# Kernel tuning notes

Hardware: AMD Instinct MI355X
Metric: run time of the kernel (lower is better)

Reference implementation:

```python
import jax, jax.numpy as jnp
import numpy as np

B, S, H = 2, 2048, 2048
NH, NKV, HD = 16, 4, 128          # query heads, kv heads, head_dim
THETA = 10000.0


def setup_inputs() -> dict:
    key = jax.random.key(0)
    ks = jax.random.split(key, 9)
    s = 0.02
    return {
        "hidden_states": jax.random.normal(ks[0], (B, S, H), jnp.float32),
        "q_w": jax.random.normal(ks[1], (NH * HD, H), jnp.float32) * s,
        "q_b": jax.random.normal(ks[2], (NH * HD,), jnp.float32) * s,
        "k_w": jax.random.normal(ks[3], (NKV * HD, H), jnp.float32) * s,
        "k_b": jax.random.normal(ks[4], (NKV * HD,), jnp.float32) * s,
        "v_w": jax.random.normal(ks[5], (NKV * HD, H), jnp.float32) * s,
        "v_b": jax.random.normal(ks[6], (NKV * HD,), jnp.float32) * s,
        "o_w": jax.random.normal(ks[7], (H, NH * HD), jnp.float32) * s,
        "o_b": jax.random.normal(ks[8], (H,), jnp.float32) * s,
    }


def _rotate_half(x):
    x1, x2 = jnp.split(x, 2, axis=-1)
    return jnp.concatenate([-x2, x1], axis=-1)


def reference(hidden_states, q_w, q_b, k_w, k_b, v_w, v_b, o_w, o_b):
    b, s, h = hidden_states.shape
    # QKV projections -> (b, heads, s, hd)
    q = (hidden_states @ q_w.T + q_b).reshape(b, s, NH, HD).transpose(0, 2, 1, 3)
    k = (hidden_states @ k_w.T + k_b).reshape(b, s, NKV, HD).transpose(0, 2, 1, 3)
    v = (hidden_states @ v_w.T + v_b).reshape(b, s, NKV, HD).transpose(0, 2, 1, 3)
    # rotary embedding (default position_ids = arange(s))
    pos = jnp.arange(s, dtype=jnp.float32)
    inv_freq = 1.0 / (THETA ** (jnp.arange(0, HD, 2, dtype=jnp.float32) / HD))
    freqs = pos[:, None] * inv_freq[None, :]          # (s, hd/2)
    emb = jnp.concatenate([freqs, freqs], axis=-1)    # (s, hd)
    cos = jnp.cos(emb)[None, None]                    # (1,1,s,hd)
    sin = jnp.sin(emb)[None, None]
    q = q * cos + _rotate_half(q) * sin
    k = k * cos + _rotate_half(k) * sin
    # GQA: repeat kv heads (repeat_interleave along head dim)
    n_rep = NH // NKV
    k = jnp.repeat(k, n_rep, axis=1)
    v = jnp.repeat(v, n_rep, axis=1)
    # attention (mathematically what the chunked online-softmax intends)
    scores = jnp.einsum('bhqd,bhkd->bhqk', q, k) / np.sqrt(HD).astype(np.float32)
    m = jnp.max(scores, axis=-1, keepdims=True)
    e = jnp.exp(scores - m)
    attn = jnp.einsum('bhqk,bhkd->bhqd', e, v) / (jnp.sum(e, axis=-1, keepdims=True) + 1e-10)
    attn = attn.transpose(0, 2, 1, 3).reshape(b, s, NH * HD)
    return attn @ o_w.T + o_b
```

## Files before the change

kernel.cpp:

```cpp
#include <hip/hip_runtime.h>
#include <hip/hip_bf16.h>
#include <math.h>

typedef __attribute__((ext_vector_type(8))) short bf16x8;
typedef __attribute__((ext_vector_type(4))) float f32x4;
typedef __attribute__((ext_vector_type(16))) float f32x16;
typedef __attribute__((ext_vector_type(4))) unsigned int u32x4;

#if __has_builtin(__builtin_amdgcn_exp2f)
#define EXP2(x) __builtin_amdgcn_exp2f(x)
#else
#define EXP2(x) __expf((x) * 0.6931471805599453f)
#endif

__device__ __forceinline__ ushort f2bf(float f) {
  unsigned u = __float_as_uint(f);
  u = u + 0x7FFFu + ((u >> 16) & 1u);
  return (ushort)(u >> 16);
}
__device__ __forceinline__ float bf2f(ushort h) {
  return __uint_as_float(((unsigned)h) << 16);
}
__device__ __forceinline__ unsigned cvtpk(float a, float b) {
  unsigned r;
  asm("v_cvt_pk_bf16_f32 %0, %1, %2" : "=v"(r) : "v"(a), "v"(b));
  return r;
}
__device__ __forceinline__ void gload_lds16(const ushort* g, ushort* l) {
  __builtin_amdgcn_global_load_lds((const __attribute__((address_space(1))) void*)g,
                                   (__attribute__((address_space(3))) void*)l, 16, 0, 0);
}

__global__ __launch_bounds__(256) void prep_kernel(
    const float* __restrict__ hs, const float* __restrict__ qw,
    const float* __restrict__ kw, const float* __restrict__ vw,
    const float* __restrict__ ow, const float* __restrict__ qb,
    const float* __restrict__ kb, const float* __restrict__ vb,
    ushort* __restrict__ hs_b, ushort* __restrict__ qkvw_b,
    ushort* __restrict__ ow_b, float* __restrict__ qkvb)
{
  const int idx = blockIdx.x * 256 + threadIdx.x;
  const int stride = gridDim.x * 256;
  const float4* hs4 = (const float4*)hs;
  const float4* qw4 = (const float4*)qw;
  const float4* kw4 = (const float4*)kw;
  const float4* vw4 = (const float4*)vw;
  const float4* ow4 = (const float4*)ow;
  ushort4* hsb4 = (ushort4*)hs_b;
  ushort4* qkvwb4 = (ushort4*)qkvw_b;
  ushort4* owb4 = (ushort4*)ow_b;

  for (int i = idx; i < 2097152; i += stride) {
    float4 v = hs4[i];
    ushort4 o; o.x=f2bf(v.x); o.y=f2bf(v.y); o.z=f2bf(v.z); o.w=f2bf(v.w);
    hsb4[i] = o;
  }
  for (int i = idx; i < 1048576; i += stride) {
    float4 v = qw4[i];
    ushort4 o; o.x=f2bf(v.x); o.y=f2bf(v.y); o.z=f2bf(v.z); o.w=f2bf(v.w);
    qkvwb4[i] = o;
  }
  for (int i = idx; i < 262144; i += stride) {
    float4 v = kw4[i];
    ushort4 o; o.x=f2bf(v.x); o.y=f2bf(v.y); o.z=f2bf(v.z); o.w=f2bf(v.w);
    qkvwb4[1048576 + i] = o;
  }
  for (int i = idx; i < 262144; i += stride) {
    float4 v = vw4[i];
    ushort4 o; o.x=f2bf(v.x); o.y=f2bf(v.y); o.z=f2bf(v.z); o.w=f2bf(v.w);
    qkvwb4[1310720 + i] = o;
  }
  for (int i = idx; i < 1048576; i += stride) {
    float4 v = ow4[i];
    ushort4 o; o.x=f2bf(v.x); o.y=f2bf(v.y); o.z=f2bf(v.z); o.w=f2bf(v.w);
    owb4[i] = o;
  }
  for (int i = idx; i < 3072; i += stride)
    qkvb[i] = (i < 2048) ? qb[i] : (i < 2560 ? kb[i - 2048] : vb[i - 2560]);
}

template<int BF16OUT>
__global__ __launch_bounds__(256) void gemm_bt(
    const ushort* __restrict__ A, const ushort* __restrict__ Bw,
    const float* __restrict__ bias, void* __restrict__ Cout,
    ushort* __restrict__ vt,
    int M, int N, int K, int ldc, int vsplit)
{
  __shared__ ushort As[128 * 32];
  __shared__ ushort Bs[128 * 32];
  const int t = threadIdx.x;
  const int wv = t >> 6;
  const int lane = t & 63;
  const int qd = lane >> 4, ln = lane & 15;
  const long row0 = (long)blockIdx.x * 128, col0 = (long)blockIdx.y * 128;
  const int wm = (wv >> 1) * 64, wn = (wv & 1) * 64;

  f32x4 acc[4][4];
#pragma unroll
  for (int i = 0; i < 4; i++)
#pragma unroll
    for (int j = 0; j < 4; j++) acc[i][j] = (f32x4){0.f, 0.f, 0.f, 0.f};

  const ushort* gA = A + (row0 + (t >> 2)) * (long)K + (t & 3) * 8;
  const ushort* gB = Bw + (col0 + (t >> 2)) * (long)K + (t & 3) * 8;
  ushort* lA = &As[wv * 512];
  ushort* lB = &Bs[wv * 512];
  const long K64 = 64l * K;

  for (int kt = 0; kt < K; kt += 32) {
    __syncthreads();
    gload_lds16(gA + kt,        lA);
    gload_lds16(gA + kt + K64,  lA + 2048);
    gload_lds16(gB + kt,        lB);
    gload_lds16(gB + kt + K64,  lB + 2048);
    __syncthreads();
    bf16x8 af[4], bf[4];
#pragma unroll
    for (int mi = 0; mi < 4; mi++)
      af[mi] = *(const bf16x8*)&As[(wm + mi * 16 + ln) * 32 + qd * 8];
#pragma unroll
    for (int ni = 0; ni < 4; ni++)
      bf[ni] = *(const bf16x8*)&Bs[(wn + ni * 16 + ln) * 32 + qd * 8];
#pragma unroll
    for (int mi = 0; mi < 4; mi++)
#pragma unroll
      for (int ni = 0; ni < 4; ni++)
        acc[mi][ni] = __builtin_amdgcn_mfma_f32_16x16x32_bf16(af[mi], bf[ni], acc[mi][ni], 0, 0, 0);
  }

  float bv[4];
#pragma unroll
  for (int ni = 0; ni < 4; ni++) bv[ni] = bias[col0 + wn + ni * 16 + ln];

  if (col0 >= vsplit) {
#pragma unroll
    for (int mi = 0; mi < 4; mi++)
#pragma unroll
      for (int ni = 0; ni < 4; ni++)
#pragma unroll
        for (int r = 0; r < 4; r++) {
          long row = row0 + wm + mi * 16 + qd * 4 + r;
          long col = col0 + wn + ni * 16 + ln - vsplit;
          vt[col * 4096 + row] = f2bf(acc[mi][ni][r] + bv[ni]);
        }
  } else {
#pragma unroll
    for (int mi = 0; mi < 4; mi++)
#pragma unroll
      for (int ni = 0; ni < 4; ni++)
#pragma unroll
        for (int r = 0; r < 4; r++) {
          long row = row0 + wm + mi * 16 + qd * 4 + r;
          long col = col0 + wn + ni * 16 + ln;
          float v = acc[mi][ni][r] + bv[ni];
          if (BF16OUT) ((ushort*)Cout)[row * ldc + col] = f2bf(v);
          else         ((float*)Cout)[row * ldc + col] = v;
        }
  }
}

__global__ __launch_bounds__(256) void rope_kernel(ushort* __restrict__ qk)
{
  const int i = blockIdx.x * 256 + threadIdx.x;
  if (i >= 5242880) return;
  const int pair = i & 63;
  const int head = (i >> 6) % 20;
  const int row  = (i >> 6) / 20;
  const int pos  = row & 2047;
  const int base = head < 16 ? head * 128 : 2048 + (head - 16) * 128;
  ushort* p = qk + (long)row * 2560 + base + pair;
  const float v0 = bf2f(p[0]);
  const float v1 = bf2f(p[64]);
  const float inv = expf((float)pair * -0.14391156831212787f);
  const float ang = (float)pos * inv;
  const float sc = (head < 16) ? 0.12751744399764505f : 1.0f;
  const float c = cosf(ang) * sc, s = sinf(ang) * sc;
  p[0]  = f2bf(v0 * c - v1 * s);
  p[64] = f2bf(v1 * c + v0 * s);
}

__global__ __launch_bounds__(256, 2) void flash_kernel(
    const ushort* __restrict__ qk, const ushort* __restrict__ vt,
    ushort* __restrict__ ctx)
{
  __shared__ ushort smem[32768];
  const int t = threadIdx.x, lane = t & 63, wv = t >> 6;
  const int h2 = lane >> 5, m = lane & 31;
  const int q0 = blockIdx.x * 128;
  const int b = blockIdx.y >> 4, h = blockIdx.y & 15;
  const long rb = (long)b * 2048;
  const ushort* Qg  = qk + (rb + q0) * 2560 + h * 128;
  const ushort* Kg  = qk + rb * 2560 + 2048 + (h >> 2) * 128;
  const ushort* Vtg = vt + ((long)(h >> 2) * 128) * 4096 + rb;

  bf16x8 qf[8];
  {
    const ushort* qrow = Qg + (long)(wv * 32 + m) * 2560 + h2 * 8;
#pragma unroll
    for (int s2 = 0; s2 < 8; s2++)
      qf[s2] = *(const bf16x8*)(qrow + s2 * 16);
  }

  f32x16 oacc[4];
#pragma unroll
  for (int d = 0; d < 4; d++)
#pragma unroll
    for (int r = 0; r < 16; r++) oacc[d][r] = 0.f;
  float l_run = 0.f;

  const ushort* gK[4];
  const ushort* gV[4];
#pragma unroll
  for (int s = 0; s < 4; s++) {
    int krow = wv * 16 + s * 4 + (lane >> 4);
    int kcd  = (lane & 15) ^ (krow & 15);
    gK[s] = Kg + (long)krow * 2560 + kcd * 8;
    int vrow = wv * 32 + s * 8 + (lane >> 3);
    int vcd  = (lane & 7) ^ ((lane >> 3) & 7);
    gV[s] = Vtg + (long)vrow * 4096 + vcd * 8;
  }
  const int ldsK = wv * 16 * 128;
  const int ldsV = 8192 + wv * 32 * 64;

#pragma unroll
  for (int s = 0; s < 4; s++) gload_lds16(gK[s], smem + ldsK + s * 512);
#pragma unroll
  for (int s = 0; s < 4; s++) gload_lds16(gV[s], smem + ldsV + s * 512);
#pragma unroll
  for (int s = 0; s < 4; s++) { gK[s] += 64l * 2560; gV[s] += 64; }

  const int mk = (m & 15) ;
  const int mv = (m & 7);

  for (int kt = 0; kt < 2048; kt += 64) {
    const int cb = (kt >> 6) & 1;
    __syncthreads();
    if (kt < 1984) {
      ushort* nb = smem + (cb ^ 1) * 16384;
#pragma unroll
      for (int s = 0; s < 4; s++) gload_lds16(gK[s], nb + ldsK + s * 512);
#pragma unroll
      for (int s = 0; s < 4; s++) gload_lds16(gV[s], nb + ldsV + s * 512);
#pragma unroll
      for (int s = 0; s < 4; s++) { gK[s] += 64l * 2560; gV[s] += 64; }
    }
    const ushort* KsB  = smem + cb * 16384;
    const ushort* VtsB = KsB + 8192;

    float s_sum = 0.f;
#pragma unroll
    for (int kb = 0; kb < 2; kb++) {
      f32x16 sacc;
#pragma unroll
      for (int r = 0; r < 16; r++) sacc[r] = 0.f;
      __builtin_amdgcn_s_setprio(1);
#pragma unroll
      for (int s2 = 0; s2 < 8; s2++) {
        bf16x8 kf = *(const bf16x8*)&KsB[(32 * kb + m) * 128 + ((s2 * 2 + h2) ^ mk) * 8];
        sacc = __builtin_amdgcn_mfma_f32_32x32x16_bf16(kf, qf[s2], sacc, 0, 0, 0);
      }
      __builtin_amdgcn_s_setprio(0);
#pragma unroll
      for (int sh = 0; sh < 2; sh++) {
        float e0 = EXP2(sacc[8 * sh + 0]);
        float e1 = EXP2(sacc[8 * sh + 1]);
        float e2 = EXP2(sacc[8 * sh + 2]);
        float e3 = EXP2(sacc[8 * sh + 3]);
        float e4 = EXP2(sacc[8 * sh + 4]);
        float e5 = EXP2(sacc[8 * sh + 5]);
        float e6 = EXP2(sacc[8 * sh + 6]);
        float e7 = EXP2(sacc[8 * sh + 7]);
        s_sum += ((e0 + e1) + (e2 + e3)) + ((e4 + e5) + (e6 + e7));
        unsigned u0 = cvtpk(e0, e1);
        unsigned u1 = cvtpk(e2, e3);
        unsigned u2 = cvtpk(e4, e5);
        unsigned u3 = cvtpk(e6, e7);
        auto r0 = __builtin_amdgcn_permlane32_swap(u0, u2, false, false);
        auto r1 = __builtin_amdgcn_permlane32_swap(u1, u3, false, false);
        u32x4 pu;
        pu.x = r0[0];
        pu.y = r1[0];
        pu.z = r0[1];
        pu.w = r1[1];
        bf16x8 pfv = __builtin_bit_cast(bf16x8, pu);
        const int s = 2 * kb + sh;
        __builtin_amdgcn_s_setprio(1);
#pragma unroll
        for (int db = 0; db < 4; db++) {
          bf16x8 vf = *(const bf16x8*)&VtsB[(db * 32 + m) * 64 + ((s * 2 + h2) ^ mv) * 8];
          oacc[db] = __builtin_amdgcn_mfma_f32_32x32x16_bf16(vf, pfv, oacc[db], 0, 0, 0);
        }
        __builtin_amdgcn_s_setprio(0);
      }
    }
    l_run += s_sum + __int_as_float(__shfl_xor(__float_as_int(s_sum), 32, 64));
  }

  const float linv = 1.f / (l_run + 1e-10f);
  __syncthreads();
  ushort* Obuf = smem;
#pragma unroll
  for (int db = 0; db < 4; db++)
#pragma unroll
    for (int r = 0; r < 16; r++) {
      int d = db * 32 + (r & 3) + 8 * (r >> 2) + 4 * h2;
      Obuf[(wv * 32 + m) * 136 + d] = f2bf(oacc[db][r] * linv);
    }
  __syncthreads();
  {
    int qr = t >> 1;
    ushort* dst = ctx + (rb + q0 + qr) * 2048 + h * 128;
#pragma unroll
    for (int c = 0; c < 8; c++) {
      int off = ((t & 1) * 8 + c) * 8;
      *(uint4*)(dst + off) = *(const uint4*)&Obuf[qr * 136 + off];
    }
  }
}

extern "C" void kernel_launch(void* const* d_in, const int* in_sizes, int n_in,
                              void* d_out, int out_size, void* d_ws, size_t ws_size,
                              hipStream_t stream)
{
  const float* hs = (const float*)d_in[0];
  const float* qw = (const float*)d_in[1];
  const float* qb = (const float*)d_in[2];
  const float* kw = (const float*)d_in[3];
  const float* kb = (const float*)d_in[4];
  const float* vw = (const float*)d_in[5];
  const float* vb = (const float*)d_in[6];
  const float* ow = (const float*)d_in[7];
  const float* ob = (const float*)d_in[8];

  char* ws = (char*)d_ws;
  ushort* hs_b   = (ushort*)(ws);
  ushort* qkvw_b = (ushort*)(ws + 16777216);
  ushort* ow_b   = (ushort*)(ws + 29360128);
  float*  qkvb   = (float*) (ws + 37748736);
  ushort* qkbuf  = (ushort*)(ws + 37761024);
  ushort* vtbuf  = (ushort*)(ws + 58732544);
  ushort* ctx    = (ushort*)(ws + 62926848);

  prep_kernel<<<1024, 256, 0, stream>>>(hs, qw, kw, vw, ow, qb, kb, vb,
                                        hs_b, qkvw_b, ow_b, qkvb);
  gemm_bt<1><<<dim3(32, 24), 256, 0, stream>>>(hs_b, qkvw_b, qkvb, qkbuf, vtbuf,
                                               4096, 3072, 2048, 2560, 2560);
  rope_kernel<<<20480, 256, 0, stream>>>(qkbuf);
  flash_kernel<<<dim3(16, 32), 256, 0, stream>>>(qkbuf, vtbuf, ctx);
  gemm_bt<0><<<dim3(32, 16), 256, 0, stream>>>(ctx, ow_b, ob, d_out, nullptr,
                                               4096, 2048, 2048, 2048, 1 << 30);
}
```

Baseline: 333.6 us.

## Fuse RoPE into QKV GEMM epilogue and remap workgroups across XCDs

Removes the separate rope kernel by computing RoPE in the QKV GEMM epilogue. Each wave now covers a full 128-wide head column tile, so both halves of a rotation pair sit in the same thread. The cos/sin table is precomputed in the prep kernel and stored in the ctx workspace region, which the flash kernel later overwrites. All three main kernels also remap block IDs so neighbouring logical tiles land on the same XCD for better L2 reuse. The costs are a different per-wave tile shape in the QKV GEMM and extra table reads in its epilogue.

```diff
diff --git a/kernel.cpp b/kernel.cpp
--- a/kernel.cpp
+++ b/kernel.cpp
@@ -37,7 +37,8 @@
     const float* __restrict__ ow, const float* __restrict__ qb,
     const float* __restrict__ kb, const float* __restrict__ vb,
     ushort* __restrict__ hs_b, ushort* __restrict__ qkvw_b,
-    ushort* __restrict__ ow_b, float* __restrict__ qkvb)
+    ushort* __restrict__ ow_b, float* __restrict__ qkvb,
+    float2* __restrict__ rope_tab)
 {
   const int idx = blockIdx.x * 256 + threadIdx.x;
   const int stride = gridDim.x * 256;
@@ -77,14 +78,18 @@
   }
   for (int i = idx; i < 3072; i += stride)
     qkvb[i] = (i < 2048) ? qb[i] : (i < 2560 ? kb[i - 2048] : vb[i - 2560]);
-}
-
-template<int BF16OUT>
-__global__ __launch_bounds__(256) void gemm_bt(
+  for (int i = idx; i < 131072; i += stride) {
+    int pos = i >> 6, d = i & 63;
+    float inv = __expf((float)d * -0.14391156831212787f);
+    float ang = (float)pos * inv;
+    rope_tab[i] = make_float2(cosf(ang), sinf(ang));
+  }
+}
+
+__global__ __launch_bounds__(256) void gemm_qkv(
     const ushort* __restrict__ A, const ushort* __restrict__ Bw,
-    const float* __restrict__ bias, void* __restrict__ Cout,
-    ushort* __restrict__ vt,
-    int M, int N, int K, int ldc, int vsplit)
+    const float* __restrict__ bias, ushort* __restrict__ qkbuf,
+    ushort* __restrict__ vt, const float2* __restrict__ tab)
 {
   __shared__ ushort As[128 * 32];
   __shared__ ushort Bs[128 * 32];
@@ -92,7 +97,99 @@
   const int wv = t >> 6;
   const int lane = t & 63;
   const int qd = lane >> 4, ln = lane & 15;
-  const long row0 = (long)blockIdx.x * 128, col0 = (long)blockIdx.y * 128;
+  const int hwid = blockIdx.x + 32 * blockIdx.y;
+  const int logical = (hwid & 7) * 96 + (hwid >> 3);
+  const long row0 = (long)(logical & 31) * 128;
+  const long col0 = (long)(logical >> 5) * 128;
+
+  f32x4 acc[2][8];
+#pragma unroll
+  for (int i = 0; i < 2; i++)
+#pragma unroll
+    for (int j = 0; j < 8; j++) acc[i][j] = (f32x4){0.f, 0.f, 0.f, 0.f};
+
+  const ushort* gA = A + (row0 + (t >> 2)) * 2048l + (t & 3) * 8;
+  const ushort* gB = Bw + (col0 + (t >> 2)) * 2048l + (t & 3) * 8;
+  ushort* lA = &As[wv * 512];
+  ushort* lB = &Bs[wv * 512];
+  const long K64 = 64l * 2048;
+
+  for (int kt = 0; kt < 2048; kt += 32) {
+    __syncthreads();
+    gload_lds16(gA + kt,        lA);
+    gload_lds16(gA + kt + K64,  lA + 2048);
+    gload_lds16(gB + kt,        lB);
+    gload_lds16(gB + kt + K64,  lB + 2048);
+    __syncthreads();
+    bf16x8 af[2], bf[8];
+#pragma unroll
+    for (int mi = 0; mi < 2; mi++)
+      af[mi] = *(const bf16x8*)&As[(wv * 32 + mi * 16 + ln) * 32 + qd * 8];
+#pragma unroll
+    for (int ni = 0; ni < 8; ni++)
+      bf[ni] = *(const bf16x8*)&Bs[(ni * 16 + ln) * 32 + qd * 8];
+#pragma unroll
+    for (int mi = 0; mi < 2; mi++)
+#pragma unroll
+      for (int ni = 0; ni < 8; ni++)
+        acc[mi][ni] = __builtin_amdgcn_mfma_f32_16x16x32_bf16(af[mi], bf[ni], acc[mi][ni], 0, 0, 0);
+  }
+
+  float bv[8];
+#pragma unroll
+  for (int ni = 0; ni < 8; ni++) bv[ni] = bias[col0 + ni * 16 + ln];
+
+  if (col0 >= 2560) {
+#pragma unroll
+    for (int mi = 0; mi < 2; mi++)
+#pragma unroll
+      for (int ni = 0; ni < 8; ni++)
+#pragma unroll
+        for (int r = 0; r < 4; r++) {
+          long row = row0 + wv * 32 + mi * 16 + qd * 4 + r;
+          long col = col0 + ni * 16 + ln - 2560;
+          vt[col * 4096 + row] = f2bf(acc[mi][ni][r] + bv[ni]);
+        }
+  } else {
+    const float sc = (col0 < 2048) ? 0.12751744399764505f : 1.0f;
+#pragma unroll
+    for (int mi = 0; mi < 2; mi++)
+#pragma unroll
+      for (int ni = 0; ni < 4; ni++) {
+        const int d = ni * 16 + ln;
+#pragma unroll
+        for (int r = 0; r < 4; r++) {
+          long row = row0 + wv * 32 + mi * 16 + qd * 4 + r;
+          int pos = (int)(row & 2047);
+          float2 cs = tab[pos * 64 + d];
+          float c = cs.x * sc, s = cs.y * sc;
+          float v0 = acc[mi][ni][r]     + bv[ni];
+          float v1 = acc[mi][ni + 4][r] + bv[ni + 4];
+          ushort* p = qkbuf + row * 2560 + col0 + d;
+          p[0]  = f2bf(v0 * c - v1 * s);
+          p[64] = f2bf(v1 * c + v0 * s);
+        }
+      }
+  }
+}
+
+__global__ __launch_bounds__(256) void gemm_bt(
+    const ushort* __restrict__ A, const ushort* __restrict__ Bw,
+    const float* __restrict__ bias, float* __restrict__ Cout,
+    int K, int ldc)
+{
+  __shared__ ushort As[128 * 32];
+  __shared__ ushort Bs[128 * 32];
+  const int t = threadIdx.x;
+  const int wv = t >> 6;
+  const int lane = t & 63;
+  const int qd = lane >> 4, ln = lane & 15;
+  const int nwg = gridDim.x * gridDim.y;
+  const int cpx = nwg >> 3;
+  const int hwid = blockIdx.x + gridDim.x * blockIdx.y;
+  const int logical = (hwid & 7) * cpx + (hwid >> 3);
+  const long row0 = (long)(logical % gridDim.x) * 128;
+  const long col0 = (long)(logical / gridDim.x) * 128;
   const int wm = (wv >> 1) * 64, wn = (wv & 1) * 64;
 
   f32x4 acc[4][4];
@@ -132,51 +229,16 @@
 #pragma unroll
   for (int ni = 0; ni < 4; ni++) bv[ni] = bias[col0 + wn + ni * 16 + ln];
 
-  if (col0 >= vsplit) {
-#pragma unroll
-    for (int mi = 0; mi < 4; mi++)
-#pragma unroll
-      for (int ni = 0; ni < 4; ni++)
-#pragma unroll
-        for (int r = 0; r < 4; r++) {
-          long row = row0 + wm + mi * 16 + qd * 4 + r;
-          long col = col0 + wn + ni * 16 + ln - vsplit;
-          vt[col * 4096 + row] = f2bf(acc[mi][ni][r] + bv[ni]);
-        }
-  } else {
-#pragma unroll
-    for (int mi = 0; mi < 4; mi++)
-#pragma unroll
-      for (int ni = 0; ni < 4; ni++)
-#pragma unroll
-        for (int r = 0; r < 4; r++) {
-          long row = row0 + wm + mi * 16 + qd * 4 + r;
-          long col = col0 + wn + ni * 16 + ln;
-          float v = acc[mi][ni][r] + bv[ni];
-          if (BF16OUT) ((ushort*)Cout)[row * ldc + col] = f2bf(v);
-          else         ((float*)Cout)[row * ldc + col] = v;
-        }
-  }
-}
-
-__global__ __launch_bounds__(256) void rope_kernel(ushort* __restrict__ qk)
-{
-  const int i = blockIdx.x * 256 + threadIdx.x;
-  if (i >= 5242880) return;
-  const int pair = i & 63;
-  const int head = (i >> 6) % 20;
-  const int row  = (i >> 6) / 20;
-  const int pos  = row & 2047;
-  const int base = head < 16 ? head * 128 : 2048 + (head - 16) * 128;
-  ushort* p = qk + (long)row * 2560 + base + pair;
-  const float v0 = bf2f(p[0]);
-  const float v1 = bf2f(p[64]);
-  const float inv = expf((float)pair * -0.14391156831212787f);
-  const float ang = (float)pos * inv;
-  const float sc = (head < 16) ? 0.12751744399764505f : 1.0f;
-  const float c = cosf(ang) * sc, s = sinf(ang) * sc;
-  p[0]  = f2bf(v0 * c - v1 * s);
-  p[64] = f2bf(v1 * c + v0 * s);
+#pragma unroll
+  for (int mi = 0; mi < 4; mi++)
+#pragma unroll
+    for (int ni = 0; ni < 4; ni++)
+#pragma unroll
+      for (int r = 0; r < 4; r++) {
+        long row = row0 + wm + mi * 16 + qd * 4 + r;
+        long col = col0 + wn + ni * 16 + ln;
+        Cout[row * ldc + col] = acc[mi][ni][r] + bv[ni];
+      }
 }
 
 __global__ __launch_bounds__(256, 2) void flash_kernel(
@@ -186,8 +248,11 @@
   __shared__ ushort smem[32768];
   const int t = threadIdx.x, lane = t & 63, wv = t >> 6;
   const int h2 = lane >> 5, m = lane & 31;
-  const int q0 = blockIdx.x * 128;
-  const int b = blockIdx.y >> 4, h = blockIdx.y & 15;
+  const int hwid = blockIdx.x + 16 * blockIdx.y;
+  const int logical = (hwid & 7) * 64 + (hwid >> 3);
+  const int bx = logical & 15, by = logical >> 4;
+  const int q0 = bx * 128;
+  const int b = by >> 4, h = by & 15;
   const long rb = (long)b * 2048;
   const ushort* Qg  = qk + (rb + q0) * 2560 + h * 128;
   const ushort* Kg  = qk + rb * 2560 + 2048 + (h >> 2) * 128;
@@ -229,7 +294,7 @@
 #pragma unroll
   for (int s = 0; s < 4; s++) { gK[s] += 64l * 2560; gV[s] += 64; }
 
-  const int mk = (m & 15) ;
+  const int mk = (m & 15);
   const int mv = (m & 7);
 
   for (int kt = 0; kt < 2048; kt += 64) {
@@ -340,13 +405,13 @@
   ushort* qkbuf  = (ushort*)(ws + 37761024);
   ushort* vtbuf  = (ushort*)(ws + 58732544);
   ushort* ctx    = (ushort*)(ws + 62926848);
+  float2* rope_tab = (float2*)(ws + 62926848);
 
   prep_kernel<<<1024, 256, 0, stream>>>(hs, qw, kw, vw, ow, qb, kb, vb,
-                                        hs_b, qkvw_b, ow_b, qkvb);
-  gemm_bt<1><<<dim3(32, 24), 256, 0, stream>>>(hs_b, qkvw_b, qkvb, qkbuf, vtbuf,
-                                               4096, 3072, 2048, 2560, 2560);
-  rope_kernel<<<20480, 256, 0, stream>>>(qkbuf);
+                                        hs_b, qkvw_b, ow_b, qkvb, rope_tab);
+  gemm_qkv<<<dim3(32, 24), 256, 0, stream>>>(hs_b, qkvw_b, qkvb, qkbuf, vtbuf,
+                                             rope_tab);
   flash_kernel<<<dim3(16, 32), 256, 0, stream>>>(qkbuf, vtbuf, ctx);
-  gemm_bt<0><<<dim3(32, 16), 256, 0, stream>>>(ctx, ow_b, ob, d_out, nullptr,
-                                               4096, 2048, 2048, 2048, 1 << 30);
-}
+  gemm_bt<<<dim3(32, 16), 256, 0, stream>>>(ctx, ow_b, ob, (float*)d_out,
+                                            2048, 2048);
+}
```

Result: slower. 343.8 us (+3.0%).

## Fuse RoPE into QKV GEMM epilogue and switch to 256x256 double-buffered GEMM

Applied to the files above, without the earlier changes.

Replaces the 128x128 GEMM with a 512-thread 256x256 tile kernel that double-buffers LDS loads, interleaves the global-to-LDS copies with MFMA work, and raises wave priority around the MFMAs. For the QKV projection, the column mapping is permuted so each wave holds both halves of a rotary pair, which lets RoPE and the Q scaling run in the epilogue and removes the separate rope pass over the QK buffer. A cos/sin table is precomputed in the prep kernel and stored in the same workspace region later used for ctx, which is safe only because the table is consumed before flash writes ctx. Larger tiles mean fewer blocks (192 and 128), which may leave CUs underused.

```diff
diff --git a/kernel.cpp b/kernel.cpp
--- a/kernel.cpp
+++ b/kernel.cpp
@@ -37,7 +37,8 @@
     const float* __restrict__ ow, const float* __restrict__ qb,
     const float* __restrict__ kb, const float* __restrict__ vb,
     ushort* __restrict__ hs_b, ushort* __restrict__ qkvw_b,
-    ushort* __restrict__ ow_b, float* __restrict__ qkvb)
+    ushort* __restrict__ ow_b, float* __restrict__ qkvb,
+    float2* __restrict__ rope_tab)
 {
   const int idx = blockIdx.x * 256 + threadIdx.x;
   const int stride = gridDim.x * 256;
@@ -77,106 +78,151 @@
   }
   for (int i = idx; i < 3072; i += stride)
     qkvb[i] = (i < 2048) ? qb[i] : (i < 2560 ? kb[i - 2048] : vb[i - 2560]);
-}
-
-template<int BF16OUT>
-__global__ __launch_bounds__(256) void gemm_bt(
+  for (int i = idx; i < 131072; i += stride) {
+    int pos = i >> 6, d = i & 63;
+    float inv = __expf((float)d * -0.14391156831212787f);
+    float ang = (float)pos * inv;
+    rope_tab[i] = make_float2(cosf(ang), sinf(ang));
+  }
+}
+
+template<int MODE>
+__global__ __launch_bounds__(512, 2) void gemm256(
     const ushort* __restrict__ A, const ushort* __restrict__ Bw,
-    const float* __restrict__ bias, void* __restrict__ Cout,
-    ushort* __restrict__ vt,
-    int M, int N, int K, int ldc, int vsplit)
+    const float* __restrict__ bias, void* __restrict__ out,
+    ushort* __restrict__ vt, const float2* __restrict__ tab)
 {
-  __shared__ ushort As[128 * 32];
-  __shared__ ushort Bs[128 * 32];
-  const int t = threadIdx.x;
-  const int wv = t >> 6;
-  const int lane = t & 63;
+  __shared__ ushort smem[32768];
+  const int tid = threadIdx.x;
+  const int lane = tid & 63, wid = tid >> 6;
+  const int wr = wid >> 2, wc = wid & 3;
   const int qd = lane >> 4, ln = lane & 15;
-  const long row0 = (long)blockIdx.x * 128, col0 = (long)blockIdx.y * 128;
-  const int wm = (wv >> 1) * 64, wn = (wv & 1) * 64;
-
-  f32x4 acc[4][4];
-#pragma unroll
-  for (int i = 0; i < 4; i++)
+  const long row0 = (long)blockIdx.x * 256, col0 = (long)blockIdx.y * 256;
+  const long K = 2048;
+
+  int pcolF[4];
+#pragma unroll
+  for (int ni = 0; ni < 4; ni++)
+    pcolF[ni] = MODE ? (8 * (wc >> 1) + 2 * (wc & 1) + (ni & 1) + (ni >> 1) * 4)
+                     : (wc * 4 + ni);
+
+  f32x4 acc[8][4];
+#pragma unroll
+  for (int i = 0; i < 8; i++)
 #pragma unroll
     for (int j = 0; j < 4; j++) acc[i][j] = (f32x4){0.f, 0.f, 0.f, 0.f};
 
-  const ushort* gA = A + (row0 + (t >> 2)) * (long)K + (t & 3) * 8;
-  const ushort* gB = Bw + (col0 + (t >> 2)) * (long)K + (t & 3) * 8;
-  ushort* lA = &As[wv * 512];
-  ushort* lB = &Bs[wv * 512];
-  const long K64 = 64l * K;
-
-  for (int kt = 0; kt < K; kt += 32) {
-    __syncthreads();
-    gload_lds16(gA + kt,        lA);
-    gload_lds16(gA + kt + K64,  lA + 2048);
-    gload_lds16(gB + kt,        lB);
-    gload_lds16(gB + kt + K64,  lB + 2048);
-    __syncthreads();
-    bf16x8 af[4], bf[4];
+  const ushort* gA = A + (row0 + (tid >> 2)) * K + (tid & 3) * 8;
+  const ushort* gB = Bw + (col0 + (tid >> 2)) * K + (tid & 3) * 8;
+  const long R128 = 128 * K;
+  const int tid8 = tid * 8;
+
+  gload_lds16(gA,        smem + tid8);
+  gload_lds16(gA + R128, smem + 4096 + tid8);
+  gload_lds16(gB,        smem + 8192 + tid8);
+  gload_lds16(gB + R128, smem + 12288 + tid8);
+
+  for (int kt = 0; kt < 2048; kt += 32) {
+    const int st = (kt >> 5) & 1;
+    const ushort* As = smem + st * 16384;
+    const ushort* Bs = As + 8192;
+    ushort* Dst = smem + (st ^ 1) * 16384;
+    const bool more = (kt + 32) < 2048;
+
+    if (more) {
+      gload_lds16(gA + kt + 32,        Dst + tid8);
+      gload_lds16(gA + kt + 32 + R128, Dst + 4096 + tid8);
+      asm volatile("s_waitcnt vmcnt(2)" ::: "memory");
+    } else {
+      asm volatile("s_waitcnt vmcnt(0)" ::: "memory");
+    }
+    __builtin_amdgcn_s_barrier();
+    asm volatile("" ::: "memory");
+    bf16x8 bf[4], af[4];
+#pragma unroll
+    for (int ni = 0; ni < 4; ni++)
+      bf[ni] = *(const bf16x8*)&Bs[(pcolF[ni] * 16 + ln) * 32 + qd * 8];
 #pragma unroll
     for (int mi = 0; mi < 4; mi++)
-      af[mi] = *(const bf16x8*)&As[(wm + mi * 16 + ln) * 32 + qd * 8];
-#pragma unroll
-    for (int ni = 0; ni < 4; ni++)
-      bf[ni] = *(const bf16x8*)&Bs[(wn + ni * 16 + ln) * 32 + qd * 8];
+      af[mi] = *(const bf16x8*)&As[(wr * 128 + mi * 16 + ln) * 32 + qd * 8];
+    __builtin_amdgcn_s_setprio(1);
 #pragma unroll
     for (int mi = 0; mi < 4; mi++)
 #pragma unroll
       for (int ni = 0; ni < 4; ni++)
         acc[mi][ni] = __builtin_amdgcn_mfma_f32_16x16x32_bf16(af[mi], bf[ni], acc[mi][ni], 0, 0, 0);
+    __builtin_amdgcn_s_setprio(0);
+
+    bf16x8 ag[4];
+#pragma unroll
+    for (int mi = 0; mi < 4; mi++)
+      ag[mi] = *(const bf16x8*)&As[(wr * 128 + 64 + mi * 16 + ln) * 32 + qd * 8];
+    if (more) {
+      gload_lds16(gB + kt + 32,        Dst + 8192 + tid8);
+      gload_lds16(gB + kt + 32 + R128, Dst + 12288 + tid8);
+    }
+    __builtin_amdgcn_s_setprio(1);
+#pragma unroll
+    for (int mi = 0; mi < 4; mi++)
+#pragma unroll
+      for (int ni = 0; ni < 4; ni++)
+        acc[mi + 4][ni] = __builtin_amdgcn_mfma_f32_16x16x32_bf16(ag[mi], bf[ni], acc[mi + 4][ni], 0, 0, 0);
+    __builtin_amdgcn_s_setprio(0);
+    asm volatile("" ::: "memory");
+    __builtin_amdgcn_s_barrier();
+    asm volatile("" ::: "memory");
   }
 
   float bv[4];
 #pragma unroll
-  for (int ni = 0; ni < 4; ni++) bv[ni] = bias[col0 + wn + ni * 16 + ln];
-
-  if (col0 >= vsplit) {
-#pragma unroll
-    for (int mi = 0; mi < 4; mi++)
+  for (int ni = 0; ni < 4; ni++) bv[ni] = bias[col0 + pcolF[ni] * 16 + ln];
+
+  if (MODE == 0) {
+    float* C = (float*)out;
+#pragma unroll
+    for (int j = 0; j < 8; j++)
 #pragma unroll
       for (int ni = 0; ni < 4; ni++)
 #pragma unroll
         for (int r = 0; r < 4; r++) {
-          long row = row0 + wm + mi * 16 + qd * 4 + r;
-          long col = col0 + wn + ni * 16 + ln - vsplit;
-          vt[col * 4096 + row] = f2bf(acc[mi][ni][r] + bv[ni]);
+          long row = row0 + wr * 128 + j * 16 + qd * 4 + r;
+          long col = col0 + pcolF[ni] * 16 + ln;
+          C[row * 2048 + col] = acc[j][ni][r] + bv[ni];
+        }
+  } else if (col0 >= 2560) {
+#pragma unroll
+    for (int j = 0; j < 8; j++)
+#pragma unroll
+      for (int ni = 0; ni < 4; ni++)
+#pragma unroll
+        for (int r = 0; r < 4; r++) {
+          long row = row0 + wr * 128 + j * 16 + qd * 4 + r;
+          long col = col0 + pcolF[ni] * 16 + ln - 2560;
+          vt[col * 4096 + row] = f2bf(acc[j][ni][r] + bv[ni]);
         }
   } else {
-#pragma unroll
-    for (int mi = 0; mi < 4; mi++)
-#pragma unroll
-      for (int ni = 0; ni < 4; ni++)
+    ushort* qkbuf = (ushort*)out;
+    const float sc = (col0 < 2048) ? 0.12751744399764505f : 1.0f;
+    const long hbase = col0 + (wc >> 1) * 128;
+#pragma unroll
+    for (int j = 0; j < 8; j++)
+#pragma unroll
+      for (int ni = 0; ni < 2; ni++) {
+        const int d = (2 * (wc & 1) + ni) * 16 + ln;
 #pragma unroll
         for (int r = 0; r < 4; r++) {
-          long row = row0 + wm + mi * 16 + qd * 4 + r;
-          long col = col0 + wn + ni * 16 + ln;
-          float v = acc[mi][ni][r] + bv[ni];
-          if (BF16OUT) ((ushort*)Cout)[row * ldc + col] = f2bf(v);
-          else         ((float*)Cout)[row * ldc + col] = v;
+          long row = row0 + wr * 128 + j * 16 + qd * 4 + r;
+          int pos = (int)(row & 2047);
+          float2 cs = tab[pos * 64 + d];
+          float c = cs.x * sc, s = cs.y * sc;
+          float v0 = acc[j][ni][r]     + bv[ni];
+          float v1 = acc[j][ni + 2][r] + bv[ni + 2];
+          ushort* p = qkbuf + row * 2560 + hbase + d;
+          p[0]  = f2bf(v0 * c - v1 * s);
+          p[64] = f2bf(v1 * c + v0 * s);
         }
-  }
-}
-
-__global__ __launch_bounds__(256) void rope_kernel(ushort* __restrict__ qk)
-{
-  const int i = blockIdx.x * 256 + threadIdx.x;
-  if (i >= 5242880) return;
-  const int pair = i & 63;
-  const int head = (i >> 6) % 20;
-  const int row  = (i >> 6) / 20;
-  const int pos  = row & 2047;
-  const int base = head < 16 ? head * 128 : 2048 + (head - 16) * 128;
-  ushort* p = qk + (long)row * 2560 + base + pair;
-  const float v0 = bf2f(p[0]);
-  const float v1 = bf2f(p[64]);
-  const float inv = expf((float)pair * -0.14391156831212787f);
-  const float ang = (float)pos * inv;
-  const float sc = (head < 16) ? 0.12751744399764505f : 1.0f;
-  const float c = cosf(ang) * sc, s = sinf(ang) * sc;
-  p[0]  = f2bf(v0 * c - v1 * s);
-  p[64] = f2bf(v1 * c + v0 * s);
+      }
+  }
 }
 
 __global__ __launch_bounds__(256, 2) void flash_kernel(
@@ -229,7 +275,7 @@
 #pragma unroll
   for (int s = 0; s < 4; s++) { gK[s] += 64l * 2560; gV[s] += 64; }
 
-  const int mk = (m & 15) ;
+  const int mk = (m & 15);
   const int mv = (m & 7);
 
   for (int kt = 0; kt < 2048; kt += 64) {
@@ -340,13 +386,13 @@
   ushort* qkbuf  = (ushort*)(ws + 37761024);
   ushort* vtbuf  = (ushort*)(ws + 58732544);
   ushort* ctx    = (ushort*)(ws + 62926848);
+  float2* rope_tab = (float2*)(ws + 62926848);
 
   prep_kernel<<<1024, 256, 0, stream>>>(hs, qw, kw, vw, ow, qb, kb, vb,
-                                        hs_b, qkvw_b, ow_b, qkvb);
-  gemm_bt<1><<<dim3(32, 24), 256, 0, stream>>>(hs_b, qkvw_b, qkvb, qkbuf, vtbuf,
-                                               4096, 3072, 2048, 2560, 2560);
-  rope_kernel<<<20480, 256, 0, stream>>>(qkbuf);
+                                        hs_b, qkvw_b, ow_b, qkvb, rope_tab);
+  gemm256<1><<<dim3(16, 12), 512, 0, stream>>>(hs_b, qkvw_b, qkvb, (void*)qkbuf,
+                                               vtbuf, rope_tab);
   flash_kernel<<<dim3(16, 32), 256, 0, stream>>>(qkbuf, vtbuf, ctx);
-  gemm_bt<0><<<dim3(32, 16), 256, 0, stream>>>(ctx, ow_b, ob, d_out, nullptr,
-                                               4096, 2048, 2048, 2048, 1 << 30);
-}
+  gemm256<0><<<dim3(16, 8), 512, 0, stream>>>(ctx, ow_b, ob, d_out,
+                                              nullptr, nullptr);
+}
```

Result: no change. 329.7 us (-1.2%).
